# Optimization experiments

Measured on AMD Instinct MI355X. Metric: run time of the kernel, lower is better.

## Reference

```python
import jax, jax.numpy as jnp
import numpy as np

VOCAB = 32000
HID = 1024
LAYERS = 2
BATCH = 16
SEQ = 256


def setup_inputs() -> dict:
    key = jax.random.key(0)
    ks = jax.random.split(key, 8)
    s = 1.0 / np.sqrt(HID)
    x = jax.random.randint(ks[0], (BATCH, SEQ), 0, VOCAB, dtype=jnp.int64)
    embed = jax.random.normal(ks[1], (VOCAB, HID), dtype=jnp.float32) * 0.02
    Wi = jax.random.uniform(ks[2], (LAYERS, HID, HID), jnp.float32, -s, s)
    bi = jax.random.uniform(ks[3], (LAYERS, HID), jnp.float32, -s, s)
    Wh = jax.random.uniform(ks[4], (LAYERS, HID, HID), jnp.float32, -s, s)
    bh = jax.random.uniform(ks[5], (LAYERS, HID), jnp.float32, -s, s)
    Wo = jax.random.uniform(ks[6], (VOCAB, HID), jnp.float32, -s, s)
    bo = jax.random.uniform(ks[7], (VOCAB,), jnp.float32, -s, s)
    return {"x": x, "embed": embed, "Wi": Wi, "bi": bi, "Wh": Wh, "bh": bh, "Wo": Wo, "bo": bo}


def reference(x, embed, Wi, bi, Wh, bh, Wo, bo):
    B, S = x.shape
    L, H, _ = Wi.shape
    emb = embed[x]                      # [B, S, H]
    emb_t = jnp.swapaxes(emb, 0, 1)     # [S, B, H]
    h0 = jnp.zeros((L, B, H), dtype=embed.dtype)

    def step(hidden, x_t):
        inp = x_t
        new_h = []
        for l in range(L):
            inp = jnp.tanh(inp @ Wi[l].T + bi[l] + hidden[l] @ Wh[l].T + bh[l])
            new_h.append(inp)
        hidden = jnp.stack(new_h)       # [L, B, H]
        return hidden, inp              # emit top-layer hidden per step

    hidden, tops = jax.lax.scan(step, h0, emb_t)   # tops: [S, B, H]
    # project all steps at once (same math as per-step fc_out)
    logits = jnp.einsum('sbh,vh->bsv', tops, Wo) + bo  # [B, S, V]
    return logits, hidden
```

## Files before the change

### kernel.cpp

```cpp
#include <hip/hip_runtime.h>
#include <cmath>
#include <cstdint>

#define VOCAB 32000
#define HID   1024
#define BATCH 16
#define SEQ   256
#define NL0   64
#define NL1   128
#define MASTER 192
#define NBLK  256
#define BH    (BATCH * HID)
#define NTILE_M 16
#define NTILE_N 125
#define NTILES  (NTILE_M * NTILE_N)

typedef __attribute__((ext_vector_type(8))) short short8;
typedef __attribute__((ext_vector_type(4))) float f32x4;

__device__ __forceinline__ ushort f2bf(float f) {
  uint u = __builtin_bit_cast(uint, f);
  return (ushort)((u + 0x7FFFu + ((u >> 16) & 1u)) >> 16);
}
__device__ __forceinline__ float bf2f(ushort h) {
  return __builtin_bit_cast(float, (uint)h << 16);
}

#define LOAD8(d, base)                                                        \
  asm volatile(                                                               \
    "global_load_dwordx4 %0, %8, off sc0 sc1\n\t"                             \
    "global_load_dwordx4 %1, %8, off offset:512 sc0 sc1\n\t"                  \
    "global_load_dwordx4 %2, %8, off offset:1024 sc0 sc1\n\t"                 \
    "global_load_dwordx4 %3, %8, off offset:1536 sc0 sc1\n\t"                 \
    "global_load_dwordx4 %4, %8, off offset:2048 sc0 sc1\n\t"                 \
    "global_load_dwordx4 %5, %8, off offset:2560 sc0 sc1\n\t"                 \
    "global_load_dwordx4 %6, %8, off offset:3072 sc0 sc1\n\t"                 \
    "global_load_dwordx4 %7, %8, off offset:3584 sc0 sc1"                     \
    : "=&v"(d[0]), "=&v"(d[1]), "=&v"(d[2]), "=&v"(d[3]),                     \
      "=&v"(d[4]), "=&v"(d[5]), "=&v"(d[6]), "=&v"(d[7])                      \
    : "v"(base) : "memory")

#define WAIT8(d)                                                              \
  asm volatile("s_waitcnt vmcnt(0)"                                           \
    : "+v"(d[0]), "+v"(d[1]), "+v"(d[2]), "+v"(d[3]),                         \
      "+v"(d[4]), "+v"(d[5]), "+v"(d[6]), "+v"(d[7]) :: "memory")

__device__ __forceinline__ void st_coherent(float* p, float v) {
  asm volatile("global_store_dword %0, %1, off sc0 sc1" :: "v"(p), "v"(v) : "memory");
}
__device__ __forceinline__ void st_coherent_u16(ushort* p, ushort v) {
  asm volatile("global_store_short %0, %1, off sc0 sc1" :: "v"(p), "v"((uint)v) : "memory");
}
__device__ __forceinline__ int ld_rlx(const int* p) {
  return __hip_atomic_load(p, __ATOMIC_RELAXED, __HIP_MEMORY_SCOPE_AGENT);
}
__device__ __forceinline__ void st_rlx(int* p, int v) {
  __hip_atomic_store(p, v, __ATOMIC_RELAXED, __HIP_MEMORY_SCOPE_AGENT);
}

__global__ __launch_bounds__(256) void pre0_gemm(
    const int* __restrict__ x, const float* __restrict__ embed,
    const float* __restrict__ Wi0, const float* __restrict__ bi0,
    const float* __restrict__ bh0, float* __restrict__ pre)
{
  __shared__ float As[32][132];
  __shared__ float Bs[32][132];
  const int tid  = threadIdx.x;
  const int n0   = blockIdx.x * 128;
  const int m0   = blockIdx.y * 128;
  const int lrow = tid >> 3, lkq = tid & 7;
  const int ty   = tid >> 4, tx  = tid & 15;

  const float* arow[4];
#pragma unroll
  for (int q = 0; q < 4; ++q) {
    int m = m0 + lrow + 32 * q;
    int t = m >> 4, b = m & 15;
    arow[q] = embed + (size_t)x[b * SEQ + t] * HID;
  }
  const float* brow = Wi0 + (size_t)(n0 + lrow) * HID;

  float acc[8][8];
#pragma unroll
  for (int i = 0; i < 8; ++i)
#pragma unroll
    for (int j = 0; j < 8; ++j) acc[i][j] = 0.f;

  for (int kt = 0; kt < HID; kt += 32) {
    float4 av[4], bv[4];
#pragma unroll
    for (int q = 0; q < 4; ++q) {
      av[q] = *(const float4*)(arow[q] + kt + lkq * 4);
      bv[q] = *(const float4*)(brow + (size_t)(32 * q) * HID + kt + lkq * 4);
    }
    __syncthreads();
#pragma unroll
    for (int q = 0; q < 4; ++q) {
      int r = lrow + 32 * q;
      As[lkq*4+0][r] = av[q].x; As[lkq*4+1][r] = av[q].y;
      As[lkq*4+2][r] = av[q].z; As[lkq*4+3][r] = av[q].w;
      Bs[lkq*4+0][r] = bv[q].x; Bs[lkq*4+1][r] = bv[q].y;
      Bs[lkq*4+2][r] = bv[q].z; Bs[lkq*4+3][r] = bv[q].w;
    }
    __syncthreads();
#pragma unroll
    for (int kk = 0; kk < 32; ++kk) {
      float4 a0 = *(const float4*)&As[kk][ty * 8];
      float4 a1 = *(const float4*)&As[kk][ty * 8 + 4];
      float4 b0 = *(const float4*)&Bs[kk][tx * 8];
      float4 b1 = *(const float4*)&Bs[kk][tx * 8 + 4];
      float a[8] = {a0.x,a0.y,a0.z,a0.w,a1.x,a1.y,a1.z,a1.w};
      float b[8] = {b0.x,b0.y,b0.z,b0.w,b1.x,b1.y,b1.z,b1.w};
#pragma unroll
      for (int i = 0; i < 8; ++i)
#pragma unroll
        for (int j = 0; j < 8; ++j) acc[i][j] = fmaf(a[i], b[j], acc[i][j]);
    }
  }

#pragma unroll
  for (int i = 0; i < 8; ++i) {
    int m = m0 + ty * 8 + i;
    float* o = pre + (size_t)m * HID + n0 + tx * 8;
#pragma unroll
    for (int j = 0; j < 8; ++j) {
      int n = n0 + tx * 8 + j;
      o[j] = acc[i][j] + bi0[n] + bh0[n];
    }
  }
}

__global__ __launch_bounds__(256) void wo_conv(
    const float* __restrict__ Wo, ushort* __restrict__ WoH)
{
  const size_t total = (size_t)VOCAB * HID;
  for (size_t i = ((size_t)blockIdx.x * 256 + threadIdx.x) * 8; i < total;
       i += (size_t)gridDim.x * 256 * 8) {
    float4 v0 = *(const float4*)(Wo + i);
    float4 v1 = *(const float4*)(Wo + i + 4);
    short8 w;
    w[0] = (short)f2bf(v0.x); w[1] = (short)f2bf(v0.y);
    w[2] = (short)f2bf(v0.z); w[3] = (short)f2bf(v0.w);
    w[4] = (short)f2bf(v1.x); w[5] = (short)f2bf(v1.y);
    w[6] = (short)f2bf(v1.z); w[7] = (short)f2bf(v1.w);
    *(short8*)(WoH + i) = w;
  }
}

__global__ __launch_bounds__(512) void rnn_scan(
    const float* __restrict__ Wi, const float* __restrict__ Wh,
    const float* __restrict__ bi, const float* __restrict__ bh,
    const float* __restrict__ pre0, float* __restrict__ h0ring,
    float* __restrict__ h1g, ushort* __restrict__ topsHi,
    ushort* __restrict__ topsLo, const float* __restrict__ Wo,
    const ushort* __restrict__ WoH, const float* __restrict__ bo,
    float* __restrict__ out, int* __restrict__ bar)
{
  __shared__ __align__(16) char pool[139328];
  __shared__ int tkt_s;
  const int tid = threadIdx.x;
  const int blk = blockIdx.x;
  const int rep = (blk & 7) * 32;
  int* go0r = bar + 12 * 32 + rep;
  int* go1r = bar + 20 * 32 + rep;
  int* ticket = bar + 28 * 32;

  auto proj_tiles = [&]() {
    ushort* Ahi = (ushort*)pool;
    ushort* Alo = Ahi + 16384;
    ushort* Bs  = Alo + 16384;
    const int lane = tid & 63, wv = tid >> 6;
    const int wm = wv & 3, wn = wv >> 2;
    const int sr8 = tid >> 3;
    const int sk8 = (tid & 7) * 8;
    for (;;) {
      if (tid == 0)
        tkt_s = __hip_atomic_fetch_add(ticket, 1, __ATOMIC_RELAXED,
                                       __HIP_MEMORY_SCOPE_AGENT);
      __syncthreads();
      const int T = tkt_s;
      if (T >= NTILES) break;
      const int mt = T / NTILE_N, nt = T % NTILE_N;
      if (tid == 0) {
        const int need = 16 * (mt + 1);
        while (ld_rlx(go1r) < need) __builtin_amdgcn_s_sleep(4);
      }
      __syncthreads();
      const int m0 = mt * 256, n0 = nt * 256;

      f32x4 acc[4][8];
#pragma unroll
      for (int i = 0; i < 4; ++i)
#pragma unroll
        for (int j = 0; j < 8; ++j) acc[i][j] = (f32x4)0.f;

      for (int kt = 0; kt < HID; kt += 64) {
        __syncthreads();
#pragma unroll
        for (int p = 0; p < 4; ++p) {
          int r = sr8 + 64 * p;
          uint off = (uint)(r * 128 + sk8 * 2) ^ (uint)((r & 7) << 4);
          *(short8*)((char*)Ahi + off) =
              *(const short8*)(topsHi + (size_t)(m0 + r) * HID + kt + sk8);
          *(short8*)((char*)Alo + off) =
              *(const short8*)(topsLo + (size_t)(m0 + r) * HID + kt + sk8);
          if (WoH) {
            *(short8*)((char*)Bs + off) =
                *(const short8*)(WoH + (size_t)(n0 + r) * HID + kt + sk8);
          } else {
            float4 v0 = *(const float4*)(Wo + (size_t)(n0 + r) * HID + kt + sk8);
            float4 v1 = *(const float4*)(Wo + (size_t)(n0 + r) * HID + kt + sk8 + 4);
            short8 w;
            w[0] = (short)f2bf(v0.x); w[1] = (short)f2bf(v0.y);
            w[2] = (short)f2bf(v0.z); w[3] = (short)f2bf(v0.w);
            w[4] = (short)f2bf(v1.x); w[5] = (short)f2bf(v1.y);
            w[6] = (short)f2bf(v1.z); w[7] = (short)f2bf(v1.w);
            *(short8*)((char*)Bs + off) = w;
          }
        }
        __syncthreads();

        const int fr = lane & 15, kg = lane >> 4;
#pragma unroll
        for (int kk = 0; kk < 2; ++kk) {
          short8 bf[8], ah[4], al[4];
#pragma unroll
          for (int nf = 0; nf < 8; ++nf) {
            int row = wn * 128 + nf * 16 + fr;
            uint off = (uint)(row * 128 + kk * 64 + kg * 16) ^ (uint)((row & 7) << 4);
            bf[nf] = *(const short8*)((const char*)Bs + off);
          }
#pragma unroll
          for (int mf = 0; mf < 4; ++mf) {
            int row = wm * 64 + mf * 16 + fr;
            uint off = (uint)(row * 128 + kk * 64 + kg * 16) ^ (uint)((row & 7) << 4);
            ah[mf] = *(const short8*)((const char*)Ahi + off);
            al[mf] = *(const short8*)((const char*)Alo + off);
          }
#pragma unroll
          for (int mf = 0; mf < 4; ++mf)
#pragma unroll
            for (int nf = 0; nf < 8; ++nf) {
              acc[mf][nf] = __builtin_amdgcn_mfma_f32_16x16x32_bf16(
                  ah[mf], bf[nf], acc[mf][nf], 0, 0, 0);
              acc[mf][nf] = __builtin_amdgcn_mfma_f32_16x16x32_bf16(
                  al[mf], bf[nf], acc[mf][nf], 0, 0, 0);
            }
        }
      }

      const int fr = lane & 15, rg = lane >> 4;
#pragma unroll
      for (int mf = 0; mf < 4; ++mf)
#pragma unroll
        for (int nf = 0; nf < 8; ++nf) {
          int n = n0 + wn * 128 + nf * 16 + fr;
          float bb = bo[n];
#pragma unroll
          for (int j = 0; j < 4; ++j) {
            int m = m0 + wm * 64 + mf * 16 + rg * 4 + j;
            int orow = (m & 15) * 256 + (m >> 4);
            out[(size_t)orow * VOCAB + n] = acc[mf][nf][j] + bb;
          }
        }
    }
  };

  if (blk >= MASTER) {
    if (blk == MASTER && tid == 0) {
      int e0 = 0, e1 = 0;
      while (e0 < SEQ || e1 < SEQ) {
        int s0 = 0, s1 = 0;
#pragma unroll
        for (int i = 0; i < 4; ++i) s0 += ld_rlx(bar + i * 32);
#pragma unroll
        for (int i = 0; i < 8; ++i) s1 += ld_rlx(bar + (4 + i) * 32);
        int n0 = s0 >> 6;
        int n1 = s1 >> 7;
        if (n0 > e0) {
          e0 = n0;
#pragma unroll
          for (int i = 0; i < 8; ++i) st_rlx(bar + (12 + i) * 32, e0);
        }
        if (n1 > e1) {
          e1 = n1;
#pragma unroll
          for (int i = 0; i < 8; ++i) st_rlx(bar + (20 + i) * 32, e1);
        }
      }
    }
    proj_tiles();
    return;
  }

  float* wT   = (float*)pool;
  float* hT   = wT + 16384;
  float* part = hT + 16384;
  float* bias = part + 2048;

  const bool isL0 = (blk < NL0);

  if (isL0) {
    const int j = blk;
#pragma unroll
    for (int p = 0; p < 8; ++p) {
      int idx = tid + 512 * p;
      int r = idx >> 8, kq = idx & 255;
      float4 v = *(const float4*)(Wh + ((size_t)(16 * j + r)) * HID + 4 * kq);
      wT[(4*kq+0)*16 + r] = v.x; wT[(4*kq+1)*16 + r] = v.y;
      wT[(4*kq+2)*16 + r] = v.z; wT[(4*kq+3)*16 + r] = v.w;
    }
  } else {
    const int j = blk - NL0;
#pragma unroll
    for (int p = 0; p < 8; ++p) {
      int idx = tid + 512 * p;
      int half = idx >> 11;
      int id2 = idx & 2047;
      int r = id2 >> 8, kq = id2 & 255;
      const float* W = (half ? Wh : Wi) + (size_t)HID * HID;
      float4 v = *(const float4*)(W + ((size_t)(8 * j + r)) * HID + 4 * kq);
      int kb = half * 1024 + 4 * kq;
      wT[(kb+0)*8 + r] = v.x; wT[(kb+1)*8 + r] = v.y;
      wT[(kb+2)*8 + r] = v.z; wT[(kb+3)*8 + r] = v.w;
    }
    if (tid < 8) bias[tid] = bi[HID + 8 * j + tid] + bh[HID + 8 * j + tid];
  }
  __syncthreads();

  const int sb  = tid & 15;
  const int skq = tid >> 4;
  auto hbase = [&](const float* src) {
    return (const float*)((const char*)src + sb * 4096 + skq * 16);
  };
  auto stage_write = [&](const f32x4* d) {
#pragma unroll
    for (int p = 0; p < 8; ++p) {
      int kq = skq + 32 * p;
#pragma unroll
      for (int c = 0; c < 4; ++c) hT[(4*kq+c)*16 + sb] = d[p][c];
    }
  };

  if (isL0) {
    const int bq = tid & 3, rq = (tid >> 2) & 3, ks = tid >> 4;
    for (int u = 0; u < SEQ; ++u) {
      float myPre = 0.f;
      if (tid < 256)
        myPre = pre0[((size_t)u * BATCH + (tid >> 4)) * HID + 16 * blk + (tid & 15)];

      if (tid == 0) {
        while (ld_rlx(go0r) < u) __builtin_amdgcn_s_sleep(1);
        const int need = u - 7;
        if (need > 0)
          while (ld_rlx(go1r) < need) __builtin_amdgcn_s_sleep(1);
      }
      __syncthreads();

      f32x4 r0[8];
      LOAD8(r0, hbase(h0ring + ((u - 1) & 7) * BH));
      WAIT8(r0);
      stage_write(r0);
      __syncthreads();

      float acc[4][4] = {{0.f}};
#pragma unroll 4
      for (int i = 0; i < 32; ++i) {
        int k = ks + 32 * i;
        float4 hv = *(const float4*)&hT[k * 16 + 4 * bq];
        float4 wv = *(const float4*)&wT[k * 16 + 4 * rq];
        float hb[4] = {hv.x, hv.y, hv.z, hv.w};
        float wr[4] = {wv.x, wv.y, wv.z, wv.w};
#pragma unroll
        for (int b_ = 0; b_ < 4; ++b_)
#pragma unroll
          for (int rj = 0; rj < 4; ++rj)
            acc[b_][rj] = fmaf(hb[b_], wr[rj], acc[b_][rj]);
      }
#pragma unroll
      for (int b_ = 0; b_ < 4; ++b_)
#pragma unroll
        for (int rj = 0; rj < 4; ++rj) {
          float v = acc[b_][rj];
          v += __shfl_xor(v, 16); v += __shfl_xor(v, 32);
          acc[b_][rj] = v;
        }
      const int w = tid >> 6;
      if ((tid & 63) < 16) {
#pragma unroll
        for (int b_ = 0; b_ < 4; ++b_)
#pragma unroll
          for (int rj = 0; rj < 4; ++rj)
            part[w * 256 + (4*bq + b_) * 16 + 4*rq + rj] = acc[b_][rj];
      }
      __syncthreads();
      if (tid < 256) {
        int b = tid >> 4, r = tid & 15;
        float s = myPre;
#pragma unroll
        for (int w2 = 0; w2 < 8; ++w2) s += part[w2 * 256 + b * 16 + r];
        st_coherent(h0ring + (u & 7) * BH + (size_t)b * HID + 16 * blk + r, tanhf(s));
      }
      asm volatile("s_waitcnt vmcnt(0)" ::: "memory");
      __syncthreads();
      if (tid == 0)
        __hip_atomic_fetch_add(bar + (blk & 3) * 32, 1,
                               __ATOMIC_RELAXED, __HIP_MEMORY_SCOPE_AGENT);
    }
  } else {
    const int bq = tid & 3, rq = (tid >> 2) & 1, ks = tid >> 3;
    for (int t = 0; t < SEQ; ++t) {
      if (tid == 0)
        while (ld_rlx(go0r) < t + 1) __builtin_amdgcn_s_sleep(1);
      __syncthreads();

      f32x4 r0[8];
      LOAD8(r0, hbase(h0ring + (t & 7) * BH));
      WAIT8(r0);
      stage_write(r0);
      __syncthreads();

      float acc[4][4] = {{0.f}};
#pragma unroll 4
      for (int i = 0; i < 16; ++i) {
        int k = ks + 64 * i;
        float4 hv = *(const float4*)&hT[k * 16 + 4 * bq];
        float4 wv = *(const float4*)&wT[k * 8 + 4 * rq];
        float hb[4] = {hv.x, hv.y, hv.z, hv.w};
        float wr[4] = {wv.x, wv.y, wv.z, wv.w};
#pragma unroll
        for (int b_ = 0; b_ < 4; ++b_)
#pragma unroll
          for (int rj = 0; rj < 4; ++rj)
            acc[b_][rj] = fmaf(hb[b_], wr[rj], acc[b_][rj]);
      }

      if (tid == 0 && t)
        while (ld_rlx(go1r) < t) __builtin_amdgcn_s_sleep(1);
      __syncthreads();

      f32x4 r1[8];
      LOAD8(r1, hbase(h1g + ((t - 1) & 1) * BH));
      WAIT8(r1);
      stage_write(r1);
      __syncthreads();

#pragma unroll 4
      for (int i = 0; i < 16; ++i) {
        int k = ks + 64 * i;
        float4 hv = *(const float4*)&hT[k * 16 + 4 * bq];
        float4 wv = *(const float4*)&wT[(1024 + k) * 8 + 4 * rq];
        float hb[4] = {hv.x, hv.y, hv.z, hv.w};
        float wr[4] = {wv.x, wv.y, wv.z, wv.w};
#pragma unroll
        for (int b_ = 0; b_ < 4; ++b_)
#pragma unroll
          for (int rj = 0; rj < 4; ++rj)
            acc[b_][rj] = fmaf(hb[b_], wr[rj], acc[b_][rj]);
      }
#pragma unroll
      for (int b_ = 0; b_ < 4; ++b_)
#pragma unroll
        for (int rj = 0; rj < 4; ++rj) {
          float v = acc[b_][rj];
          v += __shfl_xor(v, 8); v += __shfl_xor(v, 16); v += __shfl_xor(v, 32);
          acc[b_][rj] = v;
        }
      const int w = tid >> 6;
      if ((tid & 63) < 8) {
#pragma unroll
        for (int b_ = 0; b_ < 4; ++b_)
#pragma unroll
          for (int rj = 0; rj < 4; ++rj)
            part[w * 128 + (4*bq + b_) * 8 + 4*rq + rj] = acc[b_][rj];
      }
      __syncthreads();
      if (tid < 128) {
        int b = tid >> 3, r = tid & 7;
        float s = bias[r];
#pragma unroll
        for (int w2 = 0; w2 < 8; ++w2) s += part[w2 * 128 + b * 8 + r];
        int R = 8 * (blk - NL0) + r;
        float v = tanhf(s);
        ushort hi = f2bf(v);
        ushort lo = f2bf(v - bf2f(hi));
        size_t mi = ((size_t)t * BATCH + b) * HID + R;
        st_coherent_u16(topsHi + mi, hi);
        st_coherent_u16(topsLo + mi, lo);
        st_coherent(h1g + (t & 1) * BH + (size_t)b * HID + R, v);
      }
      asm volatile("s_waitcnt vmcnt(0)" ::: "memory");
      __syncthreads();
      if (tid == 0)
        __hip_atomic_fetch_add(bar + (4 + (blk & 7)) * 32, 1,
                               __ATOMIC_RELAXED, __HIP_MEMORY_SCOPE_AGENT);
    }
  }

  __syncthreads();
  proj_tiles();
}

__global__ void copy_hidden(const float* __restrict__ h0ring,
                            const ushort* __restrict__ topsHi,
                            const ushort* __restrict__ topsLo,
                            float* __restrict__ outh)
{
  int i = blockIdx.x * 256 + threadIdx.x;
  int l = i >> 14, rem = i & 16383;
  if (l == 0) {
    outh[i] = h0ring[7 * BH + rem];
  } else {
    size_t mi = (size_t)(SEQ - 1) * BH + rem;
    outh[i] = bf2f(topsHi[mi]) + bf2f(topsLo[mi]);
  }
}

extern "C" void kernel_launch(void* const* d_in, const int* in_sizes, int n_in,
                              void* d_out, int out_size, void* d_ws, size_t ws_size,
                              hipStream_t stream)
{
  const int*   x     = (const int*)d_in[0];
  const float* embed = (const float*)d_in[1];
  const float* Wi    = (const float*)d_in[2];
  const float* bi    = (const float*)d_in[3];
  const float* Wh    = (const float*)d_in[4];
  const float* bh    = (const float*)d_in[5];
  const float* Wo    = (const float*)d_in[6];
  const float* bo    = (const float*)d_in[7];
  float* out = (float*)d_out;

  char* ws = (char*)d_ws;
  float*  pre0   = (float*) (ws);
  ushort* topsHi = (ushort*)(ws + (16u << 20));
  ushort* topsLo = (ushort*)(ws + (24u << 20));
  float*  h0ring = (float*) (ws + (32u << 20));
  float*  h1g    = (float*) (ws + (32u << 20) + 524288);
  int*    bar    = (int*)   (ws + (32u << 20) + 655360);
  ushort* WoH    = (ushort*)(ws + (33u << 20));
  const size_t need_woh = (33ull << 20) + (size_t)VOCAB * HID * 2;
  const bool useWoH = ws_size >= need_woh;

  hipMemsetAsync(h0ring, 0, 659456, stream);

  pre0_gemm<<<dim3(8, 32), dim3(256), 0, stream>>>(x, embed, Wi, bi, bh, pre0);
  if (useWoH)
    wo_conv<<<dim3(2048), dim3(256), 0, stream>>>(Wo, WoH);

  const ushort* WoHArg = useWoH ? WoH : (const ushort*)nullptr;
  void* args[] = { (void*)&Wi, (void*)&Wh, (void*)&bi, (void*)&bh,
                   (void*)&pre0, (void*)&h0ring, (void*)&h1g,
                   (void*)&topsHi, (void*)&topsLo, (void*)&Wo,
                   (void*)&WoHArg, (void*)&bo, (void*)&out, (void*)&bar };
  hipLaunchCooperativeKernel((void*)rnn_scan, dim3(NBLK), dim3(512), args, 0, stream);

  copy_hidden<<<dim3(128), dim3(256), 0, stream>>>(
      h0ring, topsHi, topsLo, out + (size_t)BATCH * SEQ * VOCAB);
}
```

Baseline: 2.333 ms.

## Replace master-block barrier aggregation with per-block flags polled in parallel

Removes the dedicated master thread that summed atomic counters and rebroadcast step epochs. Each recurrent block now publishes its own step counter with a relaxed store, and consumers poll all producer flags in parallel across threads. This takes one hop of latency off every step of the serial scan, and it also frees the master block for projection tiles. Projection tiles additionally traverse N in serpentine order on alternate M rows for cache reuse of Wo. The cost is more polling traffic from many threads per block.

```diff
diff --git a/kernel.cpp b/kernel.cpp
--- a/kernel.cpp
+++ b/kernel.cpp
@@ -8,7 +8,6 @@
 #define SEQ   256
 #define NL0   64
 #define NL1   128
-#define MASTER 192
 #define NBLK  256
 #define BH    (BATCH * HID)
 #define NTILE_M 16
@@ -160,10 +159,17 @@
   __shared__ int tkt_s;
   const int tid = threadIdx.x;
   const int blk = blockIdx.x;
-  const int rep = (blk & 7) * 32;
-  int* go0r = bar + 12 * 32 + rep;
-  int* go1r = bar + 20 * 32 + rep;
-  int* ticket = bar + 28 * 32;
+  int* h0flag = bar;
+  int* h1flag = bar + 64 * 32;
+  int* ticket = bar + 192 * 32;
+
+  auto poll_flags = [&](const int* flags, int n, int tgt) {
+    if (tid < n) {
+      const int* p = flags + tid * 32;
+      while (ld_rlx(p) < tgt) __builtin_amdgcn_s_sleep(1);
+    }
+    __syncthreads();
+  };
 
   auto proj_tiles = [&]() {
     ushort* Ahi = (ushort*)pool;
@@ -180,10 +186,13 @@
       __syncthreads();
       const int T = tkt_s;
       if (T >= NTILES) break;
-      const int mt = T / NTILE_N, nt = T % NTILE_N;
-      if (tid == 0) {
+      const int mt = T / NTILE_N;
+      const int ntIdx = T % NTILE_N;
+      const int nt = (mt & 1) ? (NTILE_N - 1 - ntIdx) : ntIdx;
+      if (tid < NL1) {
+        const int* p = h1flag + tid * 32;
         const int need = 16 * (mt + 1);
-        while (ld_rlx(go1r) < need) __builtin_amdgcn_s_sleep(4);
+        while (ld_rlx(p) < need) __builtin_amdgcn_s_sleep(4);
       }
       __syncthreads();
       const int m0 = mt * 256, n0 = nt * 256;
@@ -266,29 +275,7 @@
     }
   };
 
-  if (blk >= MASTER) {
-    if (blk == MASTER && tid == 0) {
-      int e0 = 0, e1 = 0;
-      while (e0 < SEQ || e1 < SEQ) {
-        int s0 = 0, s1 = 0;
-#pragma unroll
-        for (int i = 0; i < 4; ++i) s0 += ld_rlx(bar + i * 32);
-#pragma unroll
-        for (int i = 0; i < 8; ++i) s1 += ld_rlx(bar + (4 + i) * 32);
-        int n0 = s0 >> 6;
-        int n1 = s1 >> 7;
-        if (n0 > e0) {
-          e0 = n0;
-#pragma unroll
-          for (int i = 0; i < 8; ++i) st_rlx(bar + (12 + i) * 32, e0);
-        }
-        if (n1 > e1) {
-          e1 = n1;
-#pragma unroll
-          for (int i = 0; i < 8; ++i) st_rlx(bar + (20 + i) * 32, e1);
-        }
-      }
-    }
+  if (blk >= NL0 + NL1) {
     proj_tiles();
     return;
   }
@@ -349,11 +336,13 @@
       if (tid < 256)
         myPre = pre0[((size_t)u * BATCH + (tid >> 4)) * HID + 16 * blk + (tid & 15)];
 
-      if (tid == 0) {
-        while (ld_rlx(go0r) < u) __builtin_amdgcn_s_sleep(1);
+      if (tid < NL0) {
+        const int* p = h0flag + tid * 32;
+        while (ld_rlx(p) < u) __builtin_amdgcn_s_sleep(1);
+      } else if (tid >= 64 && tid < 64 + NL1 && u >= 8) {
+        const int* p = h1flag + (tid - 64) * 32;
         const int need = u - 7;
-        if (need > 0)
-          while (ld_rlx(go1r) < need) __builtin_amdgcn_s_sleep(1);
+        while (ld_rlx(p) < need) __builtin_amdgcn_s_sleep(1);
       }
       __syncthreads();
 
@@ -403,15 +392,16 @@
       }
       asm volatile("s_waitcnt vmcnt(0)" ::: "memory");
       __syncthreads();
-      if (tid == 0)
-        __hip_atomic_fetch_add(bar + (blk & 3) * 32, 1,
-                               __ATOMIC_RELAXED, __HIP_MEMORY_SCOPE_AGENT);
+      if (tid == 0) st_rlx(h0flag + blk * 32, u + 1);
     }
   } else {
     const int bq = tid & 3, rq = (tid >> 2) & 1, ks = tid >> 3;
+    const int jj = blk - NL0;
     for (int t = 0; t < SEQ; ++t) {
-      if (tid == 0)
-        while (ld_rlx(go0r) < t + 1) __builtin_amdgcn_s_sleep(1);
+      if (tid < NL0) {
+        const int* p = h0flag + tid * 32;
+        while (ld_rlx(p) < t + 1) __builtin_amdgcn_s_sleep(1);
+      }
       __syncthreads();
 
       f32x4 r0[8];
@@ -435,8 +425,10 @@
             acc[b_][rj] = fmaf(hb[b_], wr[rj], acc[b_][rj]);
       }
 
-      if (tid == 0 && t)
-        while (ld_rlx(go1r) < t) __builtin_amdgcn_s_sleep(1);
+      if (t && tid < NL1) {
+        const int* p = h1flag + tid * 32;
+        while (ld_rlx(p) < t) __builtin_amdgcn_s_sleep(1);
+      }
       __syncthreads();
 
       f32x4 r1[8];
@@ -480,7 +472,7 @@
         float s = bias[r];
 #pragma unroll
         for (int w2 = 0; w2 < 8; ++w2) s += part[w2 * 128 + b * 8 + r];
-        int R = 8 * (blk - NL0) + r;
+        int R = 8 * jj + r;
         float v = tanhf(s);
         ushort hi = f2bf(v);
         ushort lo = f2bf(v - bf2f(hi));
@@ -491,9 +483,7 @@
       }
       asm volatile("s_waitcnt vmcnt(0)" ::: "memory");
       __syncthreads();
-      if (tid == 0)
-        __hip_atomic_fetch_add(bar + (4 + (blk & 7)) * 32, 1,
-                               __ATOMIC_RELAXED, __HIP_MEMORY_SCOPE_AGENT);
+      if (tid == 0) st_rlx(h1flag + jj * 32, t + 1);
     }
   }
 
@@ -541,7 +531,7 @@
   const size_t need_woh = (33ull << 20) + (size_t)VOCAB * HID * 2;
   const bool useWoH = ws_size >= need_woh;
 
-  hipMemsetAsync(h0ring, 0, 659456, stream);
+  hipMemsetAsync(h0ring, 0, 655360 + 32768, stream);
 
   pre0_gemm<<<dim3(8, 32), dim3(256), 0, stream>>>(x, embed, Wi, bi, bh, pre0);
   if (useWoH)
```

Measured after the change: 2.351 ms. About the same (+0.8%).
